# Optimization experiments

Hardware: AMD Instinct MI355X
Metric: run time of the kernel (lower is better)

The kernel has to match this reference:

```python
import jax, jax.numpy as jnp
import numpy as np

B, N, S, D_IN, D_OUT = 8, 8192, 8, 64, 64


def setup_inputs() -> dict:
    key = jax.random.key(0)
    ks = jax.random.split(key, 7)
    x = jax.random.normal(ks[0], (B, N, D_IN), dtype=jnp.float32)
    j_idx = jax.random.randint(ks[1], (B, N, S), 0, N, dtype=jnp.int32)
    k_idx = jax.random.randint(ks[2], (B, N, S), 0, N, dtype=jnp.int32)
    # MLP params: Linear(3d -> 2d), GELU, Linear(2d -> d_out)
    s1 = 1.0 / np.sqrt(3 * D_IN)
    s2 = 1.0 / np.sqrt(2 * D_IN)
    W1 = jax.random.uniform(ks[3], (3 * D_IN, 2 * D_IN), jnp.float32, -s1, s1)
    b1 = jax.random.uniform(ks[4], (2 * D_IN,), jnp.float32, -s1, s1)
    W2 = jax.random.uniform(ks[5], (2 * D_IN, D_OUT), jnp.float32, -s2, s2)
    b2 = jax.random.uniform(ks[6], (D_OUT,), jnp.float32, -s2, s2)
    return {"x": x, "j_idx": j_idx, "k_idx": k_idx, "W1": W1, "b1": b1, "W2": W2, "b2": b2}


def reference(x, j_idx, k_idx, W1, b1, W2, b2):
    # x: (B,N,D); j_idx/k_idx: (B,N,S) indices into N
    gather = jax.vmap(lambda xb, ib: xb[ib])  # per-batch gather -> (N,S,D)
    xj = gather(x, j_idx)                      # (B,N,S,D)
    xk = gather(x, k_idx)                      # (B,N,S,D)
    xi = jnp.broadcast_to(x[:, :, None, :], xj.shape)
    triple = jnp.concatenate([xi, xj, xk], axis=-1)  # (B,N,S,3D)
    h = jax.nn.gelu(triple @ W1 + b1, approximate=False)  # (B,N,S,2D)
    out = h @ W2 + b2                                       # (B,N,S,D_OUT)
    return out.mean(axis=2)                                 # (B,N,D_OUT)
```

## Files before the change

kernel.cpp:

```cpp
#include <hip/hip_runtime.h>
#include <stdint.h>


#define NT   4
#define NBLK 2048

typedef short  short8 __attribute__((ext_vector_type(8)));
typedef float  f32x4  __attribute__((ext_vector_type(4)));
typedef float  f32x16 __attribute__((ext_vector_type(16)));

__device__ __forceinline__ unsigned short f2bf(float f){
  union { float f; unsigned u; } a; a.f = f;
  unsigned u = a.u;
  u += 0x7fffu + ((u >> 16) & 1u);
  return (unsigned short)(u >> 16);
}
__device__ __forceinline__ float fast_gelu(float x){
  float x2 = x * x;
  float t  = __builtin_fmaf(x2, -0.1029437f, -2.3022083f);
  float p  = __builtin_amdgcn_exp2f(x * t);
  return x * __builtin_amdgcn_rcpf(1.0f + p);
}

__global__ void prep_kernel(const float* __restrict__ x, const float* __restrict__ W1,
                            const float* __restrict__ W2, short* __restrict__ xb,
                            short* __restrict__ w1f, short* __restrict__ w2f){
  int bid = blockIdx.x;
  if (bid < 2048){
    long i = (long)bid * 256 + threadIdx.x;
    const float4* p = (const float4*)(x + i * 8);
    float4 a = p[0], b = p[1];
    short8 v;
    v[0]=(short)f2bf(a.x); v[1]=(short)f2bf(a.y); v[2]=(short)f2bf(a.z); v[3]=(short)f2bf(a.w);
    v[4]=(short)f2bf(b.x); v[5]=(short)f2bf(b.y); v[6]=(short)f2bf(b.z); v[7]=(short)f2bf(b.w);
    *(short8*)(xb + i * 8) = v;
  } else if (threadIdx.x < 64){
    int f = bid - 2048, lane = threadIdx.x;
    short8 v;
    if (f < 48){
      int cb = f / 12, t = f % 12;
      #pragma unroll
      for (int j = 0; j < 8; j++)
        v[j] = (short)f2bf(W1[(t*16 + 8*(lane>>5) + j)*128 + cb*32 + (lane&31)]);
      *(short8*)(w1f + ((long)(f*64 + lane))*8) = v;
    } else {
      int g = f - 48; int w = g >> 2, q = g & 3;
      #pragma unroll
      for (int j = 0; j < 8; j++)
        v[j] = (short)f2bf(W2[(q*32 + 8*(lane>>4) + j)*64 + w*16 + (lane&15)]);
      *(short8*)(w2f + ((long)(g*64 + lane))*8) = v;
    }
  }
}

__global__ __launch_bounds__(512, 4) void ltc_main(
    const short* __restrict__ xb,  const short* __restrict__ w1f,
    const short* __restrict__ w2f, const int* __restrict__ jidx,
    const int* __restrict__ kidx,  const float* __restrict__ b1,
    const float* __restrict__ b2,  float* __restrict__ out)
{
  __shared__ short Ab[2][8704];
  __shared__ short HB[2][16 * 136];

  const int tid  = threadIdx.x;
  const int w    = tid >> 6, lane = tid & 63;
  const int cb   = w & 3,  rb  = w >> 2;
  const int l31  = lane & 31, hi = lane >> 5;
  const int l15  = lane & 15, q4 = lane >> 4;

  short8 w1v[12];
  #pragma unroll
  for (int t = 0; t < 12; t++)
    w1v[t] = *(const short8*)(w1f + ((long)((cb * 12 + t) * 64 + lane)) * 8);
  short8 w2v[4];
  #pragma unroll
  for (int q = 0; q < 4; q++)
    w2v[q] = *(const short8*)(w2f + ((long)((cb * 4 + q) * 64 + lane)) * 8);

  float b1v = b1[cb * 32 + l31];
  float b2v = b2[cb * 16 + l15];

  for (int i = tid; i < 8 * 136; i += 512){ HB[0][8*136 + i] = 0; HB[1][8*136 + i] = 0; }

  const int bid   = blockIdx.x;
  const int batch = bid & 7;
  const int T0    = batch * 1024 + (bid >> 3) * NT;
  const long tb0  = (long)T0 * 64;
  const int bbase = batch << 13;

  const int sg   = w >> 2;
  const int scp  = w & 3;
  const int t_st = sg * 32 + l31;
  const int o_g  = lane >> 5, o_c = (lane >> 2) & 7, o_r4 = lane & 3;

  const int r4l = l31 >> 3;
  const int oO  = rb * 512  + hi * 64  + r4l * 16;
  const int oJ  = 1024 + rb * 4096 + hi * 512 + l31 * 16;
  const int oK  = oJ + 8192;

  auto stage = [&](int buf, long tb, int jn, int kn){
    const short* gj = xb + (long)(bbase + jn) * 64 + (scp * 2 + hi) * 8;
    __builtin_amdgcn_global_load_lds(
        (const __attribute__((address_space(1))) unsigned int*)gj,
        (__attribute__((address_space(3))) unsigned int*)(&Ab[buf][512 + sg * 2048 + scp * 512]),
        16, 0, 0);
    const short* gk = xb + (long)(bbase + kn) * 64 + (scp * 2 + hi) * 8;
    __builtin_amdgcn_global_load_lds(
        (const __attribute__((address_space(1))) unsigned int*)gk,
        (__attribute__((address_space(3))) unsigned int*)(&Ab[buf][4608 + sg * 2048 + scp * 512]),
        16, 0, 0);
    if (w == 0){
      const short* go = xb + (long)((int)(tb >> 3) + o_g * 4 + o_r4) * 64 + o_c * 8;
      __builtin_amdgcn_global_load_lds(
          (const __attribute__((address_space(1))) unsigned int*)go,
          (__attribute__((address_space(3))) unsigned int*)(&Ab[buf][0]), 16, 0, 0);
    }
  };

  auto gemm2_store = [&](int buf, int ttp){
    f32x4 acc2 = {0.f, 0.f, 0.f, 0.f};
    #pragma unroll
    for (int q = 0; q < 4; q++){
      short8 hbf = *(const short8*)&HB[buf][l15 * 136 + q * 32 + q4 * 8];
      acc2 = __builtin_amdgcn_mfma_f32_16x16x32_bf16(hbf, w2v[q], acc2, 0, 0, 0);
    }
    if (lane < 32){
      long G = ((long)(T0 + ttp)) * 8;
      #pragma unroll
      for (int r = 0; r < 4; r++)
        out[(G + 4 * q4 + r) * 64 + cb * 16 + l15] = acc2[r] + b2v;
    }
  };

  int jn0 = jidx[tb0 + t_st], kn0 = kidx[tb0 + t_st];
  stage(0, tb0, jn0, kn0);
  int jnS = 0, knS = 0;
  if (NT > 1){ jnS = jidx[tb0 + 64 + t_st]; knS = kidx[tb0 + 64 + t_st]; }

  for (int tt = 0; tt < NT; ++tt){
    const int cur = tt & 1;
    asm volatile("s_waitcnt vmcnt(0) lgkmcnt(0)\n\ts_barrier" ::: "memory");
    if (tt + 1 < NT) stage(cur ^ 1, tb0 + (long)(tt + 1) * 64, jnS, knS);
    if (tt + 2 < NT){
      jnS = jidx[tb0 + (long)(tt + 2) * 64 + t_st];
      knS = kidx[tb0 + (long)(tt + 2) * 64 + t_st];
    }

    if (tt > 0 && w < 4) gemm2_store(cur ^ 1, tt - 1);

    const char* Abase = (const char*)&Ab[cur][0];
    f32x16 acc;
    #pragma unroll
    for (int r = 0; r < 16; r++) acc[r] = b1v;
    #pragma unroll
    for (int t = 0; t < 12; t++){
      int off;
      if (t < 4)       off = oO + t * 128;
      else if (t < 8)  off = oJ + (t - 4) * 1024;
      else             off = oK + (t - 8) * 1024;
      short8 af = *(const short8*)(Abase + off);
      acc = __builtin_amdgcn_mfma_f32_32x32x16_bf16(af, w1v[t], acc, 0, 0, 0);
    }

    #pragma unroll
    for (int o = 0; o < 4; o++){
      float s0 = fast_gelu(acc[4*o+0]);
      s0 += fast_gelu(acc[4*o+1]);
      s0 += fast_gelu(acc[4*o+2]);
      s0 += fast_gelu(acc[4*o+3]);
      float other = __shfl_xor(s0, 32);
      float hbv = (s0 + other) * 0.125f;
      if (hi == 0)
        HB[cur][(rb * 4 + o) * 136 + cb * 32 + l31] = (short)f2bf(hbv);
    }
  }

  asm volatile("s_waitcnt lgkmcnt(0)\n\ts_barrier" ::: "memory");
  if (w < 4) gemm2_store((NT - 1) & 1, NT - 1);
}

__global__ void ltc_naive(const float* __restrict__ x, const int* __restrict__ jidx,
                          const int* __restrict__ kidx, const float* __restrict__ W1,
                          const float* __restrict__ b1, const float* __restrict__ W2,
                          const float* __restrict__ b2, float* __restrict__ out)
{
  int gidx = blockIdx.x;
  int b = gidx >> 13;
  __shared__ float trip[8][192];
  __shared__ float hb[128];
  int t = threadIdx.x;
  for (int i = t; i < 8 * 192; i += 128){
    int s = i / 192, c = i - s * 192;
    int v = c >> 6, cc = c & 63;
    int src;
    if (v == 0)      src = gidx & 8191;
    else if (v == 1) src = jidx[gidx * 8 + s];
    else             src = kidx[gidx * 8 + s];
    trip[s][c] = x[((long)(b << 13) + src) * 64 + cc];
  }
  __syncthreads();
  float z[8];
  #pragma unroll
  for (int s = 0; s < 8; s++) z[s] = b1[t];
  for (int k = 0; k < 192; k++){
    float wv = W1[k * 128 + t];
    #pragma unroll
    for (int s = 0; s < 8; s++) z[s] = fmaf(trip[s][k], wv, z[s]);
  }
  float acc = 0.f;
  #pragma unroll
  for (int s = 0; s < 8; s++) acc += fast_gelu(z[s]);
  hb[t] = acc * 0.125f;
  __syncthreads();
  if (t < 64){
    float o = b2[t];
    for (int h = 0; h < 128; h++) o = fmaf(hb[h], W2[h * 64 + t], o);
    out[(long)gidx * 64 + t] = o;
  }
}

extern "C" void kernel_launch(void* const* d_in, const int* in_sizes, int n_in,
                              void* d_out, int out_size, void* d_ws, size_t ws_size,
                              hipStream_t stream) {
  const float* x   = (const float*)d_in[0];
  const int*   jix = (const int*)  d_in[1];
  const int*   kix = (const int*)  d_in[2];
  const float* W1  = (const float*)d_in[3];
  const float* b1  = (const float*)d_in[4];
  const float* W2  = (const float*)d_in[5];
  const float* b2  = (const float*)d_in[6];
  float* out = (float*)d_out;

  const size_t xb_elems  = (size_t)8 * 8192 * 64;
  const size_t w1f_elems = 48 * 64 * 8;
  const size_t w2f_elems = 16 * 64 * 8;
  const size_t need = (xb_elems + w1f_elems + w2f_elems) * sizeof(short);

  if (ws_size >= need){
    short* xb  = (short*)d_ws;
    short* w1f = xb + xb_elems;
    short* w2f = w1f + w1f_elems;
    prep_kernel<<<2112, 256, 0, stream>>>(x, W1, W2, xb, w1f, w2f);
    ltc_main<<<NBLK, 512, 0, stream>>>(xb, w1f, w2f, jix, kix, b1, b2, out);
  } else {
    ltc_naive<<<8 * 8192, 128, 0, stream>>>(x, jix, kix, W1, b1, W2, b2, out);
  }
}
```

Before: 59.73 us.

## Shrink block to 256 threads with 4-node tiles and swizzled own-row LDS

Each block now uses 4 waves that cover all 128 hidden columns for one 4-node tile (32 rows) per iteration, instead of 8 waves covering two 4-node row blocks. Blocks now run 8 iterations each, so the 2048 blocks still cover all nodes. LDS buffers shrink and the zero-padded HB rows go away, and all waves now do GEMM2. The own-row x tile is stored with an XOR swizzle to cut LDS bank conflicts. This trades half the per-block concurrency for smaller LDS use and a longer pipelined loop, and it duplicates the W1/W2 register load per wave with less reuse per block.

```diff
diff --git a/kernel.cpp b/kernel.cpp
--- a/kernel.cpp
+++ b/kernel.cpp
@@ -2,7 +2,7 @@
 #include <stdint.h>
 
 
-#define NT   4
+#define NT   8
 #define NBLK 2048
 
 typedef short  short8 __attribute__((ext_vector_type(8)));
@@ -53,64 +53,57 @@
   }
 }
 
-__global__ __launch_bounds__(512, 4) void ltc_main(
+__global__ __launch_bounds__(256, 4) void ltc_main(
     const short* __restrict__ xb,  const short* __restrict__ w1f,
     const short* __restrict__ w2f, const int* __restrict__ jidx,
     const int* __restrict__ kidx,  const float* __restrict__ b1,
     const float* __restrict__ b2,  float* __restrict__ out)
 {
-  __shared__ short Ab[2][8704];
-  __shared__ short HB[2][16 * 136];
+  __shared__ short Ab[2][4608];
+  __shared__ short HB[2][4 * 136];
 
   const int tid  = threadIdx.x;
   const int w    = tid >> 6, lane = tid & 63;
-  const int cb   = w & 3,  rb  = w >> 2;
   const int l31  = lane & 31, hi = lane >> 5;
   const int l15  = lane & 15, q4 = lane >> 4;
 
   short8 w1v[12];
   #pragma unroll
   for (int t = 0; t < 12; t++)
-    w1v[t] = *(const short8*)(w1f + ((long)((cb * 12 + t) * 64 + lane)) * 8);
+    w1v[t] = *(const short8*)(w1f + ((long)((w * 12 + t) * 64 + lane)) * 8);
   short8 w2v[4];
   #pragma unroll
   for (int q = 0; q < 4; q++)
-    w2v[q] = *(const short8*)(w2f + ((long)((cb * 4 + q) * 64 + lane)) * 8);
-
-  float b1v = b1[cb * 32 + l31];
-  float b2v = b2[cb * 16 + l15];
-
-  for (int i = tid; i < 8 * 136; i += 512){ HB[0][8*136 + i] = 0; HB[1][8*136 + i] = 0; }
+    w2v[q] = *(const short8*)(w2f + ((long)((w * 4 + q) * 64 + lane)) * 8);
+
+  float b1v = b1[w * 32 + l31];
+  float b2v = b2[w * 16 + l15];
 
   const int bid   = blockIdx.x;
   const int batch = bid & 7;
-  const int T0    = batch * 1024 + (bid >> 3) * NT;
-  const long tb0  = (long)T0 * 64;
+  const int tile0 = batch * 2048 + (bid >> 3) * NT;
+  const long tb0  = (long)tile0 * 32;
   const int bbase = batch << 13;
 
-  const int sg   = w >> 2;
-  const int scp  = w & 3;
-  const int t_st = sg * 32 + l31;
-  const int o_g  = lane >> 5, o_c = (lane >> 2) & 7, o_r4 = lane & 3;
-
-  const int r4l = l31 >> 3;
-  const int oO  = rb * 512  + hi * 64  + r4l * 16;
-  const int oJ  = 1024 + rb * 4096 + hi * 512 + l31 * 16;
-  const int oK  = oJ + 8192;
+  const int o_r = (lane >> 3) & 3;
+  const int o_c = (lane & 7) ^ o_r;
+
+  const int rown = l31 >> 3;
+  const int oOb  = rown * 128;
+  const int oJ   = 1024 + hi * 512 + l31 * 16;
+  const int oK   = oJ + 4096;
 
   auto stage = [&](int buf, long tb, int jn, int kn){
-    const short* gj = xb + (long)(bbase + jn) * 64 + (scp * 2 + hi) * 8;
+    const short* gj = xb + (long)(bbase + jn) * 64 + (2 * w + hi) * 8;
     __builtin_amdgcn_global_load_lds(
         (const __attribute__((address_space(1))) unsigned int*)gj,
-        (__attribute__((address_space(3))) unsigned int*)(&Ab[buf][512 + sg * 2048 + scp * 512]),
-        16, 0, 0);
-    const short* gk = xb + (long)(bbase + kn) * 64 + (scp * 2 + hi) * 8;
+        (__attribute__((address_space(3))) unsigned int*)(&Ab[buf][512 + w * 512]), 16, 0, 0);
+    const short* gk = xb + (long)(bbase + kn) * 64 + (2 * w + hi) * 8;
     __builtin_amdgcn_global_load_lds(
         (const __attribute__((address_space(1))) unsigned int*)gk,
-        (__attribute__((address_space(3))) unsigned int*)(&Ab[buf][4608 + sg * 2048 + scp * 512]),
-        16, 0, 0);
+        (__attribute__((address_space(3))) unsigned int*)(&Ab[buf][2560 + w * 512]), 16, 0, 0);
     if (w == 0){
-      const short* go = xb + (long)((int)(tb >> 3) + o_g * 4 + o_r4) * 64 + o_c * 8;
+      const short* go = xb + (long)((int)(tb >> 3) + o_r) * 64 + o_c * 8;
       __builtin_amdgcn_global_load_lds(
           (const __attribute__((address_space(1))) unsigned int*)go,
           (__attribute__((address_space(3))) unsigned int*)(&Ab[buf][0]), 16, 0, 0);
@@ -121,32 +114,32 @@
     f32x4 acc2 = {0.f, 0.f, 0.f, 0.f};
     #pragma unroll
     for (int q = 0; q < 4; q++){
-      short8 hbf = *(const short8*)&HB[buf][l15 * 136 + q * 32 + q4 * 8];
+      short8 hbf = *(const short8*)((const char*)&HB[buf][0] + (l15 & 3) * 272 + q * 64 + q4 * 16);
       acc2 = __builtin_amdgcn_mfma_f32_16x16x32_bf16(hbf, w2v[q], acc2, 0, 0, 0);
     }
-    if (lane < 32){
-      long G = ((long)(T0 + ttp)) * 8;
+    if (lane < 16){
+      long Gn = ((long)(tile0 + ttp)) * 4;
       #pragma unroll
       for (int r = 0; r < 4; r++)
-        out[(G + 4 * q4 + r) * 64 + cb * 16 + l15] = acc2[r] + b2v;
+        out[(Gn + r) * 64 + w * 16 + l15] = acc2[r] + b2v;
     }
   };
 
-  int jn0 = jidx[tb0 + t_st], kn0 = kidx[tb0 + t_st];
+  int jn0 = jidx[tb0 + l31], kn0 = kidx[tb0 + l31];
   stage(0, tb0, jn0, kn0);
   int jnS = 0, knS = 0;
-  if (NT > 1){ jnS = jidx[tb0 + 64 + t_st]; knS = kidx[tb0 + 64 + t_st]; }
+  if (NT > 1){ jnS = jidx[tb0 + 32 + l31]; knS = kidx[tb0 + 32 + l31]; }
 
   for (int tt = 0; tt < NT; ++tt){
     const int cur = tt & 1;
     asm volatile("s_waitcnt vmcnt(0) lgkmcnt(0)\n\ts_barrier" ::: "memory");
-    if (tt + 1 < NT) stage(cur ^ 1, tb0 + (long)(tt + 1) * 64, jnS, knS);
+    if (tt + 1 < NT) stage(cur ^ 1, tb0 + (long)(tt + 1) * 32, jnS, knS);
     if (tt + 2 < NT){
-      jnS = jidx[tb0 + (long)(tt + 2) * 64 + t_st];
-      knS = kidx[tb0 + (long)(tt + 2) * 64 + t_st];
-    }
-
-    if (tt > 0 && w < 4) gemm2_store(cur ^ 1, tt - 1);
+      jnS = jidx[tb0 + (long)(tt + 2) * 32 + l31];
+      knS = kidx[tb0 + (long)(tt + 2) * 32 + l31];
+    }
+
+    if (tt > 0) gemm2_store(cur ^ 1, tt - 1);
 
     const char* Abase = (const char*)&Ab[cur][0];
     f32x16 acc;
@@ -155,7 +148,7 @@
     #pragma unroll
     for (int t = 0; t < 12; t++){
       int off;
-      if (t < 4)       off = oO + t * 128;
+      if (t < 4)       off = oOb + (((2*t + hi) ^ rown) << 4);
       else if (t < 8)  off = oJ + (t - 4) * 1024;
       else             off = oK + (t - 8) * 1024;
       short8 af = *(const short8*)(Abase + off);
@@ -171,12 +164,12 @@
       float other = __shfl_xor(s0, 32);
       float hbv = (s0 + other) * 0.125f;
       if (hi == 0)
-        HB[cur][(rb * 4 + o) * 136 + cb * 32 + l31] = (short)f2bf(hbv);
+        HB[cur][o * 136 + w * 32 + l31] = (short)f2bf(hbv);
     }
   }
 
   asm volatile("s_waitcnt lgkmcnt(0)\n\ts_barrier" ::: "memory");
-  if (w < 4) gemm2_store((NT - 1) & 1, NT - 1);
+  gemm2_store((NT - 1) & 1, NT - 1);
 }
 
 __global__ void ltc_naive(const float* __restrict__ x, const int* __restrict__ jidx,
@@ -241,7 +234,7 @@
     short* w1f = xb + xb_elems;
     short* w2f = w1f + w1f_elems;
     prep_kernel<<<2112, 256, 0, stream>>>(x, W1, W2, xb, w1f, w2f);
-    ltc_main<<<NBLK, 512, 0, stream>>>(xb, w1f, w2f, jix, kix, b1, b2, out);
+    ltc_main<<<NBLK, 256, 0, stream>>>(xb, w1f, w2f, jix, kix, b1, b2, out);
   } else {
     ltc_naive<<<8 * 8192, 128, 0, stream>>>(x, jix, kix, W1, b1, W2, b2, out);
   }
```

After: 56.46 us. -5.5%, faster.
